# Performance work log

Measured on AMD Instinct MI355X. Metric: run time of the kernel, lower is better.

## Reference

```python
import jax, jax.numpy as jnp
import numpy as np

ALPHA = 0.025
BETA = 0.00025
V_TH = 1.0
EXP_TAU = 50.0          # tau_v / dt
T_NOW = 10.0            # current simulation step counter self.t
REFRAC_STEPS = 2        # refractory_period / dt
INV_TAU_V = float(np.exp(-1.0 / 50.0))   # exp(-dt/tau_v)
INV_TAU_I = float(np.exp(-1.0))          # exp(-dt/tau_i)
INV_TAU_V_PAIR = INV_TAU_V               # tau_v_pair defaults to tau_v
INV_TAU_I_PAIR = INV_TAU_I               # tau_i_pair defaults to tau_i

B, N = 32, 4096


def setup_inputs() -> dict:
    key = jax.random.key(0)
    ks = jax.random.split(key, 8)
    return {
        "inp": jax.random.normal(ks[0], (B, N), jnp.float32),
        "W_rec": jax.random.uniform(ks[1], (N, N), jnp.float32),  # nonneg dense adjacency weights
        "mem_pot": jax.random.normal(ks[2], (B, N), jnp.float32),
        "mem_cur": jax.random.normal(ks[3], (B, N), jnp.float32),
        "mem_pot_paired": jax.random.normal(ks[4], (B, N), jnp.float32),
        "mem_cur_paired": jax.random.normal(ks[5], (B, N), jnp.float32),
        "st": jnp.zeros((N,), jnp.float32),
        "refrac_neurons": jax.random.randint(ks[6], (B, N), 0, 3, jnp.int32),
    }


def reference(inp, W_rec, mem_pot, mem_cur, mem_pot_paired, mem_cur_paired, st, refrac_neurons):
    sign_mask = W_rec > 0  # torch: sign(W_rec) > 0 (weights are nonneg)

    # decrement refractory counters
    refrac = jnp.where(refrac_neurons > 0, refrac_neurons - 1, refrac_neurons)

    # threshold (ceil+clamp -> {0,1} spikes)
    S = jnp.clip(jnp.ceil(mem_pot - V_TH), 0.0, 1.0)                     # (B,N)
    S_paired = jnp.clip(jnp.ceil(mem_pot_paired - V_TH - ALPHA), 0.0, 1.0)

    # ---- plasticity weight update ----
    sp_max = S_paired.max(axis=0)            # (N,)
    st_new = jnp.where(S > 0, T_NOW, st)     # broadcasts (N,) -> (B,N), as in torch
    max_st = st_new.max(axis=0)              # (N,)
    # meshgrid(a,b) with ij indexing: |a-b|[i,j] = |max_st[i]-max_st[j]|
    diff = jnp.abs(max_st[:, None] - max_st[None, :])                    # (N,N)
    update_mask = (sp_max[:, None] > 0) & sign_mask                      # (N,N)
    updated = W_rec + BETA - jnp.where(update_mask,
                                       ALPHA * jnp.exp(diff / EXP_TAU),
                                       0.0)
    updated = jnp.clip(updated, 0.0, 1.0)
    W_new = jnp.where(sign_mask, updated, W_rec)

    # ---- integrate ----
    active = refrac == 0
    mem_cur_n = jnp.where(active, inp + S @ W_new + mem_cur, mem_cur)
    mem_cur_p_n = jnp.where(active, S @ W_new.T + mem_cur_paired, mem_cur_paired)
    mem_pot_n = jnp.where(active, mem_cur_n + mem_pot, mem_pot)
    mem_pot_p_n = jnp.where(active, mem_cur_p_n + mem_pot_paired, mem_pot_paired)

    # leak
    mem_pot_n = mem_pot_n * INV_TAU_V
    mem_cur_n = mem_cur_n * INV_TAU_I
    mem_pot_p_n = mem_pot_p_n * INV_TAU_V_PAIR
    mem_cur_p_n = mem_cur_p_n * INV_TAU_I_PAIR

    # reset spiked neurons
    mem_pot_n = jnp.where(S > 0, 0.0, mem_pot_n)
    mem_pot_p_n = jnp.where(S_paired > 0, 0.0, mem_pot_p_n)
    refrac_new = jnp.where(S > 0, REFRAC_STEPS, refrac)

    return S, mem_pot_n, W_new, mem_cur_n, mem_pot_p_n, mem_cur_p_n, refrac_new
```

## Files before the change

kernel.cpp:

```cpp
#include <hip/hip_runtime.h>
#include <cstdint>
#include <cstddef>

constexpr int N = 4096;
constexpr int B = 32;
constexpr int BN = B * N;
constexpr size_t NN = (size_t)N * N;

constexpr int TI = 256;
constexpr int TJ = 128;
constexpr int NIT = N / TI;
constexpr int NJT = N / TJ;
constexpr int ISUB = 64;
constexpr int LDT = TJ + 8;

constexpr float ALPHA = 0.025f;
constexpr float BETA = 0.00025f;
constexpr float T_NOW = 10.0f;
constexpr float INV_EXP_TAU = 0.02f;
constexpr float INV_TAU_V = 0.98019867f;
constexpr float INV_TAU_I = 0.36787944f;

typedef __attribute__((ext_vector_type(8))) short short8;
typedef __attribute__((ext_vector_type(4))) float f32x4;

__device__ inline unsigned short f2bf(float f) {
  uint32_t u = __float_as_uint(f);
  u += 0x7FFFu + ((u >> 16) & 1u);
  return (unsigned short)(u >> 16);
}

__device__ inline float wupd(float w, float mrow, float frow, float mcol) {
  float d = fabsf(mrow - mcol);
  float u = w + BETA - frow * __expf(d * INV_EXP_TAU);
  u = fminf(fmaxf(u, 0.0f), 1.0f);
  return (w > 0.0f) ? u : w;
}

__global__ __launch_bounds__(256) void pass_a(
    const float* __restrict__ mem_pot, const float* __restrict__ mem_pot_p,
    const float* __restrict__ st, float* __restrict__ S_out,
    unsigned short* __restrict__ S_bf,
    uint32_t* __restrict__ maskS, uint32_t* __restrict__ maskSP,
    float* __restrict__ max_st, float* __restrict__ rowfac) {
  int j = blockIdx.x * blockDim.x + threadIdx.x;
  if (j >= N) return;
  float stj = st[j];
  uint32_t ms = 0u, msp = 0u;
  float maxv = -3.0e38f;
  #pragma unroll
  for (int b = 0; b < B; ++b) {
    float p = mem_pot[b * N + j];
    float pp = mem_pot_p[b * N + j];
    bool s = (p - 1.0f) > 0.0f;
    bool sp = ((pp - 1.0f) - ALPHA) > 0.0f;
    S_out[b * N + j] = s ? 1.0f : 0.0f;
    S_bf[b * N + j] = s ? 0x3F80u : 0u;
    ms |= (uint32_t)s << b;
    msp |= (uint32_t)sp << b;
    maxv = fmaxf(maxv, s ? T_NOW : stj);
  }
  maskS[j] = ms;
  maskSP[j] = msp;
  max_st[j] = maxv;
  rowfac[j] = msp ? ALPHA : 0.0f;
}

__global__ __launch_bounds__(512, 4) void pass_fused(
    const float* __restrict__ W, const unsigned short* __restrict__ S_bf,
    const float* __restrict__ max_st, const float* __restrict__ rowfac,
    float* __restrict__ Wout, float* __restrict__ partSW,
    float* __restrict__ partSWT) {
  __shared__ __align__(16) unsigned short tile[ISUB * LDT];
  __shared__ float mstI[TI];
  __shared__ float facI[TI];
  __shared__ float mstJ[TJ];

  int tid = threadIdx.x;
  int wv = tid >> 6;
  int lane = tid & 63;
  int quad = lane >> 4;
  int nl = lane & 15;
  int jt = blockIdx.x;
  int it = blockIdx.y;
  int i0 = it * TI;
  int j0 = jt * TJ;

  uint32_t* tileU32 = (uint32_t*)tile;

  if (tid < TI) {
    mstI[tid] = max_st[i0 + tid];
    facI[tid] = rowfac[i0 + tid];
  } else if (tid < TI + TJ) {
    mstJ[tid - TI] = max_st[j0 + (tid - TI)];
  }

  float4 pf0, pf1, pf2, pf3;
  int row = tid >> 5;
  int c4 = tid & 31;
  {
    const float* base = W + (size_t)(i0 + row) * N + j0 + c4 * 4;
    pf0 = *(const float4*)(base);
    pf1 = *(const float4*)(base + (size_t)16 * N);
    pf2 = *(const float4*)(base + (size_t)32 * N);
    pf3 = *(const float4*)(base + (size_t)48 * N);
  }
  __syncthreads();

  f32x4 accA0 = {0.f, 0.f, 0.f, 0.f}, accA1 = {0.f, 0.f, 0.f, 0.f};
  f32x4 accB0 = {0.f, 0.f, 0.f, 0.f}, accB1 = {0.f, 0.f, 0.f, 0.f};

  for (int isub = 0; isub < TI / ISUB; ++isub) {
    float4 mj = *(const float4*)(mstJ + c4 * 4);
    #pragma unroll
    for (int p = 0; p < 4; ++p) {
      float4 w4 = (p == 0) ? pf0 : (p == 1) ? pf1 : (p == 2) ? pf2 : pf3;
      int r = p * 16 + row;
      int ig = i0 + isub * ISUB + r;
      float mi = mstI[isub * ISUB + r];
      float fi = facI[isub * ISUB + r];
      float4 u;
      u.x = wupd(w4.x, mi, fi, mj.x);
      u.y = wupd(w4.y, mi, fi, mj.y);
      u.z = wupd(w4.z, mi, fi, mj.z);
      u.w = wupd(w4.w, mi, fi, mj.w);
      *(float4*)(Wout + (size_t)ig * N + j0 + c4 * 4) = u;
      uint32_t d0 = (uint32_t)f2bf(u.x) | ((uint32_t)f2bf(u.y) << 16);
      uint32_t d1 = (uint32_t)f2bf(u.z) | ((uint32_t)f2bf(u.w) << 16);
      uint2 dd; dd.x = d0; dd.y = d1;
      *(uint2*)&tileU32[r * (LDT / 2) + c4 * 2] = dd;
    }
    if (isub + 1 < TI / ISUB) {
      const float* base =
          W + (size_t)(i0 + (isub + 1) * ISUB + row) * N + j0 + c4 * 4;
      pf0 = *(const float4*)(base);
      pf1 = *(const float4*)(base + (size_t)16 * N);
      pf2 = *(const float4*)(base + (size_t)32 * N);
      pf3 = *(const float4*)(base + (size_t)48 * N);
    }
    __syncthreads();

    if (wv < 4) {
      int js0 = wv * 2, js1 = wv * 2 + 1;
      #pragma unroll
      for (int kstep = 0; kstep < 2; ++kstep) {
        int kl = kstep * 32 + quad * 8;
        int kglob = i0 + isub * ISUB + kl;
        short8 a0 = *(const short8*)(S_bf + (size_t)nl * N + kglob);
        short8 a1 = *(const short8*)(S_bf + (size_t)(nl + 16) * N + kglob);
        short8 b0, b1;
        #pragma unroll
        for (int e = 0; e < 8; ++e) {
          b0[e] = (short)tile[(kl + e) * LDT + js0 * 16 + nl];
          b1[e] = (short)tile[(kl + e) * LDT + js1 * 16 + nl];
        }
        accA0 = __builtin_amdgcn_mfma_f32_16x16x32_bf16(a0, b0, accA0, 0, 0, 0);
        accA1 = __builtin_amdgcn_mfma_f32_16x16x32_bf16(a1, b0, accA1, 0, 0, 0);
        accB0 = __builtin_amdgcn_mfma_f32_16x16x32_bf16(a0, b1, accB0, 0, 0, 0);
        accB1 = __builtin_amdgcn_mfma_f32_16x16x32_bf16(a1, b1, accB1, 0, 0, 0);
      }
    } else {
      int ws = wv - 4;
      int il = ws * 16 + nl;
      f32x4 g0 = {0.f, 0.f, 0.f, 0.f}, g1 = {0.f, 0.f, 0.f, 0.f};
      #pragma unroll
      for (int kstep = 0; kstep < 4; ++kstep) {
        int kl = kstep * 32 + quad * 8;
        int kglobJ = j0 + kl;
        short8 a0 = *(const short8*)(S_bf + (size_t)nl * N + kglobJ);
        short8 a1 = *(const short8*)(S_bf + (size_t)(nl + 16) * N + kglobJ);
        short8 bfr = *(const short8*)&tile[il * LDT + kl];
        g0 = __builtin_amdgcn_mfma_f32_16x16x32_bf16(a0, bfr, g0, 0, 0, 0);
        g1 = __builtin_amdgcn_mfma_f32_16x16x32_bf16(a1, bfr, g1, 0, 0, 0);
      }
      int iglob = i0 + isub * ISUB + il;
      size_t basew = (size_t)jt * BN + iglob;
      #pragma unroll
      for (int r = 0; r < 4; ++r) {
        partSWT[basew + (size_t)(quad * 4 + r) * N] = g0[r];
        partSWT[basew + (size_t)(16 + quad * 4 + r) * N] = g1[r];
      }
    }
    if (isub + 1 < TI / ISUB) __syncthreads();
  }

  if (wv < 4) {
    int jg0 = j0 + (wv * 2) * 16 + nl;
    int jg1 = j0 + (wv * 2 + 1) * 16 + nl;
    size_t baseit = (size_t)it * BN;
    #pragma unroll
    for (int r = 0; r < 4; ++r) {
      partSW[baseit + (size_t)(quad * 4 + r) * N + jg0] = accA0[r];
      partSW[baseit + (size_t)(16 + quad * 4 + r) * N + jg0] = accA1[r];
      partSW[baseit + (size_t)(quad * 4 + r) * N + jg1] = accB0[r];
      partSW[baseit + (size_t)(16 + quad * 4 + r) * N + jg1] = accB1[r];
    }
  }
}

__global__ __launch_bounds__(256) void pass_d(
    const float* __restrict__ inp, const float* __restrict__ mem_pot,
    const float* __restrict__ mem_cur, const float* __restrict__ mem_pot_p,
    const float* __restrict__ mem_cur_p, const int* __restrict__ refrac_in,
    const uint32_t* __restrict__ maskS, const uint32_t* __restrict__ maskSP,
    const float* __restrict__ partSW, const float* __restrict__ partSWT,
    float* __restrict__ pot_out, float* __restrict__ cur_out,
    float* __restrict__ potp_out, float* __restrict__ curp_out,
    float* __restrict__ refrac_out) {
  int e = blockIdx.x * 256 + threadIdx.x;
  int b = e >> 12;
  int j = e & (N - 1);

  float SW = 0.0f, SWT = 0.0f;
  #pragma unroll
  for (int c = 0; c < NIT; ++c) SW += partSW[(size_t)c * BN + e];
  #pragma unroll
  for (int c = 0; c < NJT; ++c) SWT += partSWT[(size_t)c * BN + e];

  int r = refrac_in[e];
  int rd = (r > 0) ? (r - 1) : r;
  bool active = (rd == 0);
  bool s = (maskS[j] >> b) & 1u;
  bool sp = (maskSP[j] >> b) & 1u;
  float cur = mem_cur[e], pot = mem_pot[e];
  float curp = mem_cur_p[e], potp = mem_pot_p[e];

  float cur_n = active ? (inp[e] + SW + cur) : cur;
  float curp_n = active ? (SWT + curp) : curp;
  float pot_n = active ? (cur_n + pot) : pot;
  float potp_n = active ? (curp_n + potp) : potp;

  pot_n *= INV_TAU_V;
  cur_n *= INV_TAU_I;
  potp_n *= INV_TAU_V;
  curp_n *= INV_TAU_I;

  if (s) pot_n = 0.0f;
  if (sp) potp_n = 0.0f;
  int rn = s ? 2 : rd;

  pot_out[e] = pot_n;
  cur_out[e] = cur_n;
  potp_out[e] = potp_n;
  curp_out[e] = curp_n;
  refrac_out[e] = (float)rn;
}

extern "C" void kernel_launch(void* const* d_in, const int* in_sizes, int n_in,
                              void* d_out, int out_size, void* d_ws, size_t ws_size,
                              hipStream_t stream) {
  const float* inp = (const float*)d_in[0];
  const float* W = (const float*)d_in[1];
  const float* mem_pot = (const float*)d_in[2];
  const float* mem_cur = (const float*)d_in[3];
  const float* mem_pot_p = (const float*)d_in[4];
  const float* mem_cur_p = (const float*)d_in[5];
  const float* st = (const float*)d_in[6];
  const int* refrac = (const int*)d_in[7];

  float* out = (float*)d_out;
  float* S_out = out;
  float* pot_out = out + BN;
  float* W_out = out + 2 * (size_t)BN;
  float* cur_out = W_out + NN;
  float* potp_out = cur_out + BN;
  float* curp_out = potp_out + BN;
  float* refrac_out = curp_out + BN;

  uint32_t* maskS = (uint32_t*)d_ws;
  uint32_t* maskSP = maskS + N;
  float* max_st = (float*)(maskSP + N);
  float* rowfac = max_st + N;
  unsigned short* S_bf = (unsigned short*)(rowfac + N);
  float* partSW = (float*)(S_bf + BN);
  float* partSWT = partSW + (size_t)NIT * BN;

  pass_a<<<N / 256, 256, 0, stream>>>(mem_pot, mem_pot_p, st, S_out, S_bf,
                                      maskS, maskSP, max_st, rowfac);
  pass_fused<<<dim3(NJT, NIT), 512, 0, stream>>>(W, S_bf, max_st, rowfac,
                                                 W_out, partSW, partSWT);
  pass_d<<<BN / 256, 256, 0, stream>>>(inp, mem_pot, mem_cur, mem_pot_p,
                                       mem_cur_p, refrac, maskS, maskSP,
                                       partSW, partSWT, pot_out, cur_out,
                                       potp_out, curp_out, refrac_out);
}
```

Before: 156.0 us.

## Halve row tile, use 256-thread blocks with register-preloaded spike fragments

Shrinks the row tile of the fused weight-update and matmul kernel from 256 to 128 rows and the block from 512 to 256 threads. Three waves now share the eight S@W column tiles and one wave computes the S@W^T partials. Each thread prefetches eight W rows per subtile, loads the bf16 spike A-fragments into registers once instead of per k-step, and writes updated weights with nontemporal stores. The aim is better occupancy, less redundant global traffic and less cache pollution. In exchange the number of row tiles doubles, so the S@W partial buffer and the reduction work in the final pass both double.

```diff
diff --git a/kernel.cpp b/kernel.cpp
--- a/kernel.cpp
+++ b/kernel.cpp
@@ -7,7 +7,7 @@
 constexpr int BN = B * N;
 constexpr size_t NN = (size_t)N * N;
 
-constexpr int TI = 256;
+constexpr int TI = 128;
 constexpr int TJ = 128;
 constexpr int NIT = N / TI;
 constexpr int NJT = N / TJ;
@@ -66,7 +66,7 @@
   rowfac[j] = msp ? ALPHA : 0.0f;
 }
 
-__global__ __launch_bounds__(512, 4) void pass_fused(
+__global__ __launch_bounds__(256, 3) void pass_fused(
     const float* __restrict__ W, const unsigned short* __restrict__ S_bf,
     const float* __restrict__ max_st, const float* __restrict__ rowfac,
     float* __restrict__ Wout, float* __restrict__ partSW,
@@ -88,112 +88,131 @@
 
   uint32_t* tileU32 = (uint32_t*)tile;
 
+  int row8 = tid >> 5;
+  int c4 = tid & 31;
+
+  float4 pf[8];
+  {
+    const float* base = W + (size_t)(i0 + row8) * N + j0 + c4 * 4;
+    #pragma unroll
+    for (int p = 0; p < 8; ++p)
+      pf[p] = *(const float4*)(base + (size_t)(p * 8) * N);
+  }
+
   if (tid < TI) {
     mstI[tid] = max_st[i0 + tid];
     facI[tid] = rowfac[i0 + tid];
-  } else if (tid < TI + TJ) {
+  } else {
     mstJ[tid - TI] = max_st[j0 + (tid - TI)];
   }
 
-  float4 pf0, pf1, pf2, pf3;
-  int row = tid >> 5;
-  int c4 = tid & 31;
-  {
-    const float* base = W + (size_t)(i0 + row) * N + j0 + c4 * 4;
-    pf0 = *(const float4*)(base);
-    pf1 = *(const float4*)(base + (size_t)16 * N);
-    pf2 = *(const float4*)(base + (size_t)32 * N);
-    pf3 = *(const float4*)(base + (size_t)48 * N);
+  short8 aG0[4], aG1[4], aJ0[4], aJ1[4];
+  if (wv < 3) {
+    #pragma unroll
+    for (int c = 0; c < 4; ++c) {
+      aG0[c] = *(const short8*)(S_bf + (size_t)nl * N + i0 + c * 32 + quad * 8);
+      aG1[c] = *(const short8*)(S_bf + (size_t)(nl + 16) * N + i0 + c * 32 + quad * 8);
+    }
+  } else {
+    #pragma unroll
+    for (int c = 0; c < 4; ++c) {
+      aJ0[c] = *(const short8*)(S_bf + (size_t)nl * N + j0 + c * 32 + quad * 8);
+      aJ1[c] = *(const short8*)(S_bf + (size_t)(nl + 16) * N + j0 + c * 32 + quad * 8);
+    }
   }
   __syncthreads();
 
-  f32x4 accA0 = {0.f, 0.f, 0.f, 0.f}, accA1 = {0.f, 0.f, 0.f, 0.f};
-  f32x4 accB0 = {0.f, 0.f, 0.f, 0.f}, accB1 = {0.f, 0.f, 0.f, 0.f};
-
+  f32x4 accG0[3], accG1[3];
+  #pragma unroll
+  for (int t = 0; t < 3; ++t) {
+    accG0[t] = (f32x4){0.f, 0.f, 0.f, 0.f};
+    accG1[t] = (f32x4){0.f, 0.f, 0.f, 0.f};
+  }
+
+  #pragma unroll
   for (int isub = 0; isub < TI / ISUB; ++isub) {
     float4 mj = *(const float4*)(mstJ + c4 * 4);
     #pragma unroll
-    for (int p = 0; p < 4; ++p) {
-      float4 w4 = (p == 0) ? pf0 : (p == 1) ? pf1 : (p == 2) ? pf2 : pf3;
-      int r = p * 16 + row;
+    for (int p = 0; p < 8; ++p) {
+      int r = p * 8 + row8;
       int ig = i0 + isub * ISUB + r;
       float mi = mstI[isub * ISUB + r];
       float fi = facI[isub * ISUB + r];
-      float4 u;
-      u.x = wupd(w4.x, mi, fi, mj.x);
-      u.y = wupd(w4.y, mi, fi, mj.y);
-      u.z = wupd(w4.z, mi, fi, mj.z);
-      u.w = wupd(w4.w, mi, fi, mj.w);
-      *(float4*)(Wout + (size_t)ig * N + j0 + c4 * 4) = u;
-      uint32_t d0 = (uint32_t)f2bf(u.x) | ((uint32_t)f2bf(u.y) << 16);
-      uint32_t d1 = (uint32_t)f2bf(u.z) | ((uint32_t)f2bf(u.w) << 16);
+      f32x4 u;
+      u[0] = wupd(pf[p].x, mi, fi, mj.x);
+      u[1] = wupd(pf[p].y, mi, fi, mj.y);
+      u[2] = wupd(pf[p].z, mi, fi, mj.z);
+      u[3] = wupd(pf[p].w, mi, fi, mj.w);
+      __builtin_nontemporal_store(u, (f32x4*)(Wout + (size_t)ig * N + j0 + c4 * 4));
+      uint32_t d0 = (uint32_t)f2bf(u[0]) | ((uint32_t)f2bf(u[1]) << 16);
+      uint32_t d1 = (uint32_t)f2bf(u[2]) | ((uint32_t)f2bf(u[3]) << 16);
       uint2 dd; dd.x = d0; dd.y = d1;
       *(uint2*)&tileU32[r * (LDT / 2) + c4 * 2] = dd;
     }
     if (isub + 1 < TI / ISUB) {
       const float* base =
-          W + (size_t)(i0 + (isub + 1) * ISUB + row) * N + j0 + c4 * 4;
-      pf0 = *(const float4*)(base);
-      pf1 = *(const float4*)(base + (size_t)16 * N);
-      pf2 = *(const float4*)(base + (size_t)32 * N);
-      pf3 = *(const float4*)(base + (size_t)48 * N);
+          W + (size_t)(i0 + (isub + 1) * ISUB + row8) * N + j0 + c4 * 4;
+      #pragma unroll
+      for (int p = 0; p < 8; ++p)
+        pf[p] = *(const float4*)(base + (size_t)(p * 8) * N);
     }
     __syncthreads();
 
-    if (wv < 4) {
-      int js0 = wv * 2, js1 = wv * 2 + 1;
+    if (wv < 3) {
       #pragma unroll
-      for (int kstep = 0; kstep < 2; ++kstep) {
-        int kl = kstep * 32 + quad * 8;
-        int kglob = i0 + isub * ISUB + kl;
-        short8 a0 = *(const short8*)(S_bf + (size_t)nl * N + kglob);
-        short8 a1 = *(const short8*)(S_bf + (size_t)(nl + 16) * N + kglob);
-        short8 b0, b1;
-        #pragma unroll
-        for (int e = 0; e < 8; ++e) {
-          b0[e] = (short)tile[(kl + e) * LDT + js0 * 16 + nl];
-          b1[e] = (short)tile[(kl + e) * LDT + js1 * 16 + nl];
+      for (int t = 0; t < 3; ++t) {
+        int js = wv + 3 * t;
+        if (js < 8) {
+          #pragma unroll
+          for (int kstep = 0; kstep < 2; ++kstep) {
+            int kl = kstep * 32 + quad * 8;
+            int c = isub * 2 + kstep;
+            short8 b;
+            #pragma unroll
+            for (int e = 0; e < 8; ++e)
+              b[e] = (short)tile[(kl + e) * LDT + js * 16 + nl];
+            accG0[t] = __builtin_amdgcn_mfma_f32_16x16x32_bf16(aG0[c], b, accG0[t], 0, 0, 0);
+            accG1[t] = __builtin_amdgcn_mfma_f32_16x16x32_bf16(aG1[c], b, accG1[t], 0, 0, 0);
+          }
         }
-        accA0 = __builtin_amdgcn_mfma_f32_16x16x32_bf16(a0, b0, accA0, 0, 0, 0);
-        accA1 = __builtin_amdgcn_mfma_f32_16x16x32_bf16(a1, b0, accA1, 0, 0, 0);
-        accB0 = __builtin_amdgcn_mfma_f32_16x16x32_bf16(a0, b1, accB0, 0, 0, 0);
-        accB1 = __builtin_amdgcn_mfma_f32_16x16x32_bf16(a1, b1, accB1, 0, 0, 0);
       }
     } else {
-      int ws = wv - 4;
-      int il = ws * 16 + nl;
-      f32x4 g0 = {0.f, 0.f, 0.f, 0.f}, g1 = {0.f, 0.f, 0.f, 0.f};
       #pragma unroll
-      for (int kstep = 0; kstep < 4; ++kstep) {
-        int kl = kstep * 32 + quad * 8;
-        int kglobJ = j0 + kl;
-        short8 a0 = *(const short8*)(S_bf + (size_t)nl * N + kglobJ);
-        short8 a1 = *(const short8*)(S_bf + (size_t)(nl + 16) * N + kglobJ);
-        short8 bfr = *(const short8*)&tile[il * LDT + kl];
-        g0 = __builtin_amdgcn_mfma_f32_16x16x32_bf16(a0, bfr, g0, 0, 0, 0);
-        g1 = __builtin_amdgcn_mfma_f32_16x16x32_bf16(a1, bfr, g1, 0, 0, 0);
+      for (int g = 0; g < 4; ++g) {
+        int il = g * 16 + nl;
+        f32x4 g0 = {0.f, 0.f, 0.f, 0.f}, g1 = {0.f, 0.f, 0.f, 0.f};
+        #pragma unroll
+        for (int kstep = 0; kstep < 4; ++kstep) {
+          int kl = kstep * 32 + quad * 8;
+          short8 bfr = *(const short8*)&tile[il * LDT + kl];
+          g0 = __builtin_amdgcn_mfma_f32_16x16x32_bf16(aJ0[kstep], bfr, g0, 0, 0, 0);
+          g1 = __builtin_amdgcn_mfma_f32_16x16x32_bf16(aJ1[kstep], bfr, g1, 0, 0, 0);
+        }
+        int iglob = i0 + isub * ISUB + il;
+        size_t basew = (size_t)jt * BN + iglob;
+        #pragma unroll
+        for (int r = 0; r < 4; ++r) {
+          partSWT[basew + (size_t)(quad * 4 + r) * N] = g0[r];
+          partSWT[basew + (size_t)(16 + quad * 4 + r) * N] = g1[r];
+        }
       }
-      int iglob = i0 + isub * ISUB + il;
-      size_t basew = (size_t)jt * BN + iglob;
-      #pragma unroll
-      for (int r = 0; r < 4; ++r) {
-        partSWT[basew + (size_t)(quad * 4 + r) * N] = g0[r];
-        partSWT[basew + (size_t)(16 + quad * 4 + r) * N] = g1[r];
+    }
+    if (isub + 1 < TI / ISUB) __syncthreads();
+  }
+
+  if (wv < 3) {
+    size_t baseit = (size_t)it * BN;
+    #pragma unroll
+    for (int t = 0; t < 3; ++t) {
+      int js = wv + 3 * t;
+      if (js < 8) {
+        int jg = j0 + js * 16 + nl;
+        #pragma unroll
+        for (int r = 0; r < 4; ++r) {
+          partSW[baseit + (size_t)(quad * 4 + r) * N + jg] = accG0[t][r];
+          partSW[baseit + (size_t)(16 + quad * 4 + r) * N + jg] = accG1[t][r];
+        }
       }
-    }
-    if (isub + 1 < TI / ISUB) __syncthreads();
-  }
-
-  if (wv < 4) {
-    int jg0 = j0 + (wv * 2) * 16 + nl;
-    int jg1 = j0 + (wv * 2 + 1) * 16 + nl;
-    size_t baseit = (size_t)it * BN;
-    #pragma unroll
-    for (int r = 0; r < 4; ++r) {
-      partSW[baseit + (size_t)(quad * 4 + r) * N + jg0] = accA0[r];
-      partSW[baseit + (size_t)(16 + quad * 4 + r) * N + jg0] = accA1[r];
-      partSW[baseit + (size_t)(quad * 4 + r) * N + jg1] = accB0[r];
-      partSW[baseit + (size_t)(16 + quad * 4 + r) * N + jg1] = accB1[r];
     }
   }
 }
@@ -277,7 +296,7 @@
 
   pass_a<<<N / 256, 256, 0, stream>>>(mem_pot, mem_pot_p, st, S_out, S_bf,
                                       maskS, maskSP, max_st, rowfac);
-  pass_fused<<<dim3(NJT, NIT), 512, 0, stream>>>(W, S_bf, max_st, rowfac,
+  pass_fused<<<dim3(NJT, NIT), 256, 0, stream>>>(W, S_bf, max_st, rowfac,
                                                  W_out, partSW, partSWT);
   pass_d<<<BN / 256, 256, 0, stream>>>(inp, mem_pot, mem_cur, mem_pot_p,
                                        mem_cur_p, refrac, maskS, maskSP,
```

Result: slower. 161.8 us (+3.7%).
